# Performance work log

Measured on AMD Instinct MI355X. Metric: run time of the kernel, lower is better.

The kernel has to match this reference:

```python
import jax, jax.numpy as jnp
import numpy as np

N_POINTS = 2_000_000
GRID_SIZE = (256, 256, 256)


def setup_inputs() -> dict:
    key = jax.random.key(0)
    k1, k2 = jax.random.split(key)
    size = jnp.array(GRID_SIZE, dtype=jnp.float32)
    # points uniformly covering the grid so all are valid
    x = jax.random.uniform(k1, (N_POINTS, 3), dtype=jnp.float32) * (size - 1.0)
    grid = jax.random.normal(k2, GRID_SIZE, dtype=jnp.float32)
    lower = jnp.zeros((3,), dtype=jnp.float32)
    resolution = jnp.ones((3,), dtype=jnp.float32)
    return {"x": x, "grid": grid, "lower": lower, "resolution": resolution}


def _corner_mask():
    # mask[k, j] = bit j of corner index k (8 corners of a unit cube)
    return (jnp.arange(8)[:, None] & (1 << jnp.arange(3))[None, :]) != 0  # [8,3] bool


def reference(x, grid, lower, resolution):
    # x: [N,3] points; grid: [nx,ny,nz] learned reflectance grid
    size = jnp.array(grid.shape, dtype=x.dtype)
    index = (x - lower) / resolution                                   # [N,3]
    valid = jnp.all((index >= 0) & (index <= size - 1), axis=-1)       # [N]

    lo = jnp.floor(index)
    hi = jnp.ceil(index)
    mask = _corner_mask()                                              # [8,3]

    # corner coordinates: pick ceil where mask bit set, else floor
    corners = jnp.where(mask[None], hi[:, None, :], lo[:, None, :])    # [N,8,3]
    ci = corners.astype(jnp.int32)
    values = grid[ci[..., 0], ci[..., 1], ci[..., 2]]                  # [N,8] gather

    # weight of each corner = product of distances to the OPPOSITE corner
    opposite = jnp.where(mask[None], lo[:, None, :], hi[:, None, :])   # [N,8,3]
    dist = jnp.abs(opposite - index[:, None, :])                       # [N,8,3]
    dist = dist + (dist == 0).astype(dist.dtype)  # degenerate (integer-coord) axes
    weights = jnp.prod(dist, axis=-1)                                  # [N,8]

    out = jnp.sum(values * weights, axis=-1) / jnp.sum(weights, axis=-1)  # [N]
    return jnp.where(valid, out, jnp.zeros((), dtype=out.dtype))
```

## Files before the change

### kernel.cpp

```cpp
#include <hip/hip_runtime.h>


#define NBINS 1024
#define SPTS 4096
#define SPPT 8

#define RX 17
#define RYZ 1089
#define RN (RX * RYZ)

#define ITHREADS 1024
#define CSTRIDE 16

__device__ __forceinline__ float interp_one(float ix, float iy, float iz,
                                            const float* __restrict__ g,
                                            bool& valid) {
    valid = (ix >= 0.0f) && (ix <= 255.0f) &&
            (iy >= 0.0f) && (iy <= 255.0f) &&
            (iz >= 0.0f) && (iz <= 255.0f);
    if (!valid) return 0.0f;

    float flx = floorf(ix), fcx = ceilf(ix);
    float fly = floorf(iy), fcy = ceilf(iy);
    float flz = floorf(iz), fcz = ceilf(iz);

    int x0 = (int)flx, x1 = (int)fcx;
    int y0 = (int)fly, y1 = (int)fcy;
    int z0 = (int)flz, z1 = (int)fcz;

    float wsx = ix - flx; if (wsx == 0.0f) wsx = 1.0f;
    float wux = fcx - ix; if (wux == 0.0f) wux = 1.0f;
    float wsy = iy - fly; if (wsy == 0.0f) wsy = 1.0f;
    float wuy = fcy - iy; if (wuy == 0.0f) wuy = 1.0f;
    float wsz = iz - flz; if (wsz == 0.0f) wsz = 1.0f;
    float wuz = fcz - iz; if (wuz == 0.0f) wuz = 1.0f;

    int bx0 = x0 << 16, bx1 = x1 << 16;
    int by0 = y0 << 8,  by1 = y1 << 8;

    float v0 = g[bx0 + by0 + z0];  float w0 = wux * wuy * wuz;
    float v1 = g[bx1 + by0 + z0];  float w1 = wsx * wuy * wuz;
    float v2 = g[bx0 + by1 + z0];  float w2 = wux * wsy * wuz;
    float v3 = g[bx1 + by1 + z0];  float w3 = wsx * wsy * wuz;
    float v4 = g[bx0 + by0 + z1];  float w4 = wux * wuy * wsz;
    float v5 = g[bx1 + by0 + z1];  float w5 = wsx * wuy * wsz;
    float v6 = g[bx0 + by1 + z1];  float w6 = wux * wsy * wsz;
    float v7 = g[bx1 + by1 + z1];  float w7 = wsx * wsy * wsz;

    float num = v0 * w0 + v1 * w1 + v2 * w2 + v3 * w3 +
                v4 * w4 + v5 * w5 + v6 * w6 + v7 * w7;
    float den = w0 + w1 + w2 + w3 + w4 + w5 + w6 + w7;
    return num / den;
}

__device__ __forceinline__ unsigned bin_key(float ix, float iy, float iz) {
    ix = fminf(fmaxf(ix, 0.0f), 255.0f);
    iy = fminf(fmaxf(iy, 0.0f), 255.0f);
    iz = fminf(fmaxf(iz, 0.0f), 255.0f);
    int bx = ((int)ix) >> 4;
    int by = ((int)iy) >> 5;
    int bz = ((int)iz) >> 5;
    return (unsigned)((bx << 6) | (by << 3) | bz);
}

__global__ __launch_bounds__(256) void simplegrid_direct(
    const float* __restrict__ x, const float* __restrict__ grid,
    const float* __restrict__ lower, const float* __restrict__ res,
    float* __restrict__ out, int n)
{
    int i = blockIdx.x * blockDim.x + threadIdx.x;
    if (i >= n) return;
    float ix = (x[3 * i + 0] - lower[0]) / res[0];
    float iy = (x[3 * i + 1] - lower[1]) / res[1];
    float iz = (x[3 * i + 2] - lower[2]) / res[2];
    bool valid;
    float v = interp_one(ix, iy, iz, grid, valid);
    out[i] = valid ? v : 0.0f;
}

__global__ __launch_bounds__(512) void init_cursor_kernel(
    unsigned* __restrict__ cursor, unsigned cap)
{
    int t = blockIdx.x * 512 + threadIdx.x;
    if (t < NBINS) cursor[(size_t)t * CSTRIDE] = (unsigned)t * cap;
}

__global__ __launch_bounds__(512) void scatter_kernel(
    const float* __restrict__ x, const float* __restrict__ lower,
    const float* __restrict__ res, unsigned* __restrict__ cursor,
    float* __restrict__ p3, unsigned* __restrict__ posbuf, int n)
{
    __shared__ float sxl[SPTS], syl[SPTS], szl[SPTS];
    __shared__ unsigned short kyl[SPTS];
    __shared__ unsigned cnt[NBINS], pfx[NBINS], lcur[NBINS], gbase[NBINS];
    __shared__ unsigned wsum[8];

    int t = threadIdx.x;
    int lane = t & 63, wave = t >> 6;
    cnt[2 * t] = 0u; cnt[2 * t + 1] = 0u;
    __syncthreads();

    float l0 = lower[0], l1 = lower[1], l2 = lower[2];
    float r0 = res[0],   r1 = res[1],   r2 = res[2];
    int base = blockIdx.x * SPTS;

    float px[SPPT], py[SPPT], pz[SPPT];
    unsigned key[SPPT];
    #pragma unroll
    for (int k = 0; k < SPPT; ++k) {
        int p = base + k * 512 + t;
        if (p < n) {
            px[k] = (x[3 * p + 0] - l0) / r0;
            py[k] = (x[3 * p + 1] - l1) / r1;
            pz[k] = (x[3 * p + 2] - l2) / r2;
            key[k] = bin_key(px[k], py[k], pz[k]);
            atomicAdd(&cnt[key[k]], 1u);
        }
    }
    __syncthreads();

    unsigned h = ((unsigned)blockIdx.x * 131u) & (NBINS - 1);
    unsigned b0 = (2u * t + h) & (NBINS - 1);
    unsigned b1 = (2u * t + 1u + h) & (NBINS - 1);
    unsigned cb0 = cnt[b0], cb1 = cnt[b1];
    if (cb0) gbase[b0] = atomicAdd(&cursor[(size_t)b0 * CSTRIDE], cb0);
    if (cb1) gbase[b1] = atomicAdd(&cursor[(size_t)b1 * CSTRIDE], cb1);

    unsigned c0 = cnt[2 * t], c1 = cnt[2 * t + 1];
    unsigned v = c0 + c1;
    unsigned s = v;
    #pragma unroll
    for (int off = 1; off < 64; off <<= 1) {
        unsigned u = __shfl_up(s, off);
        if (lane >= off) s += u;
    }
    if (lane == 63) wsum[wave] = s;
    __syncthreads();
    unsigned woff = 0, tot = 0;
    #pragma unroll
    for (int w = 0; w < 8; ++w) { if (w < wave) woff += wsum[w]; tot += wsum[w]; }
    unsigned excl = woff + s - v;
    pfx[2 * t] = excl;          lcur[2 * t] = excl;
    pfx[2 * t + 1] = excl + c0; lcur[2 * t + 1] = excl + c0;
    __syncthreads();

    #pragma unroll
    for (int k = 0; k < SPPT; ++k) {
        int p = base + k * 512 + t;
        if (p < n) {
            unsigned lp = atomicAdd(&lcur[key[k]], 1u);
            sxl[lp] = px[k]; syl[lp] = py[k]; szl[lp] = pz[k];
            kyl[lp] = (unsigned short)key[k];
            posbuf[p] = gbase[key[k]] + (lp - pfx[key[k]]);
        }
    }
    __syncthreads();

    for (unsigned q = t; q < tot; q += 512) {
        unsigned kk = kyl[q];
        unsigned dst = gbase[kk] + (q - pfx[kk]);
        size_t b3 = (size_t)dst * 3;
        p3[b3 + 0] = sxl[q];
        p3[b3 + 1] = syl[q];
        p3[b3 + 2] = szl[q];
    }
}

__global__ __launch_bounds__(ITHREADS) void interp_lds_kernel(
    const float* __restrict__ p3, const float* __restrict__ grid,
    const unsigned* __restrict__ cursor, float* __restrict__ osort,
    unsigned cap)
{
    extern __shared__ float lds[];
    int b = blockIdx.x;
    int t = threadIdx.x;
    int bx0 = (b >> 6) << 4;
    int by0 = ((b >> 3) & 7) << 5;
    int bz0 = (b & 7) << 5;

    for (int i = t; i < RN; i += ITHREADS) {
        int lx = i / RYZ;
        int r  = i - lx * RYZ;
        int ly = r / 33;
        int lz = r - ly * 33;
        int gx = bx0 + lx; if (gx > 255) gx = 255;
        int gy = by0 + ly; if (gy > 255) gy = 255;
        int gz = bz0 + lz; if (gz > 255) gz = 255;
        lds[i] = grid[(gx << 16) + (gy << 8) + gz];
    }
    __syncthreads();

    float fbx = (float)bx0, fby = (float)by0, fbz = (float)bz0;
    unsigned start = (unsigned)b * cap;
    unsigned end   = cursor[(size_t)b * CSTRIDE];

    for (unsigned j = start + t; j < end; j += ITHREADS) {
        size_t b3 = (size_t)j * 3;
        float ix = p3[b3 + 0], iy = p3[b3 + 1], iz = p3[b3 + 2];
        bool valid = (ix >= 0.0f) && (ix <= 255.0f) &&
                     (iy >= 0.0f) && (iy <= 255.0f) &&
                     (iz >= 0.0f) && (iz <= 255.0f);
        float fx = fminf(fmaxf(ix, 0.0f), 255.0f) - fbx;
        float fy = fminf(fmaxf(iy, 0.0f), 255.0f) - fby;
        float fz = fminf(fmaxf(iz, 0.0f), 255.0f) - fbz;

        float flx = floorf(fx), fcx = ceilf(fx);
        float fly = floorf(fy), fcy = ceilf(fy);
        float flz = floorf(fz), fcz = ceilf(fz);
        int x0 = (int)flx, x1 = (int)fcx;
        int y0 = (int)fly, y1 = (int)fcy;
        int z0 = (int)flz, z1 = (int)fcz;

        float wsx = fx - flx; if (wsx == 0.0f) wsx = 1.0f;
        float wux = fcx - fx; if (wux == 0.0f) wux = 1.0f;
        float wsy = fy - fly; if (wsy == 0.0f) wsy = 1.0f;
        float wuy = fcy - fy; if (wuy == 0.0f) wuy = 1.0f;
        float wsz = fz - flz; if (wsz == 0.0f) wsz = 1.0f;
        float wuz = fcz - fz; if (wuz == 0.0f) wuz = 1.0f;

        int ax0 = x0 * RYZ, ax1 = x1 * RYZ;
        int ay0 = y0 * 33,  ay1 = y1 * 33;

        float v0 = lds[ax0 + ay0 + z0];  float w0 = wux * wuy * wuz;
        float v1 = lds[ax1 + ay0 + z0];  float w1 = wsx * wuy * wuz;
        float v2 = lds[ax0 + ay1 + z0];  float w2 = wux * wsy * wuz;
        float v3 = lds[ax1 + ay1 + z0];  float w3 = wsx * wsy * wuz;
        float v4 = lds[ax0 + ay0 + z1];  float w4 = wux * wuy * wsz;
        float v5 = lds[ax1 + ay0 + z1];  float w5 = wsx * wuy * wsz;
        float v6 = lds[ax0 + ay1 + z1];  float w6 = wux * wsy * wsz;
        float v7 = lds[ax1 + ay1 + z1];  float w7 = wsx * wsy * wsz;

        float num = v0 * w0 + v1 * w1 + v2 * w2 + v3 * w3 +
                    v4 * w4 + v5 * w5 + v6 * w6 + v7 * w7;
        float den = w0 + w1 + w2 + w3 + w4 + w5 + w6 + w7;
        osort[j] = valid ? (num / den) : 0.0f;
    }
}

__global__ __launch_bounds__(256) void permute_kernel(
    const float* __restrict__ out_sorted, const unsigned* __restrict__ pos,
    float* __restrict__ out, int n)
{
    int i = blockIdx.x * blockDim.x + threadIdx.x;
    if (i < n) out[i] = out_sorted[pos[i]];
}

extern "C" void kernel_launch(void* const* d_in, const int* in_sizes, int n_in,
                              void* d_out, int out_size, void* d_ws, size_t ws_size,
                              hipStream_t stream) {
    const float* x     = (const float*)d_in[0];
    const float* grid  = (const float*)d_in[1];
    const float* lower = (const float*)d_in[2];
    const float* res   = (const float*)d_in[3];
    float* out = (float*)d_out;

    int n = in_sizes[0] / 3;
    int blocks_pt = (n + 255) / 256;

    size_t fixed = (size_t)NBINS * CSTRIDE * 4 + (size_t)n * 4;
    unsigned cap = 0;
    if (ws_size > fixed) {
        size_t c = (ws_size - fixed) / ((size_t)NBINS * 16);
        cap = (unsigned)(c > 8192 ? 8192 : c);
    }

    bool lds_ok = (hipFuncSetAttribute(
        (const void*)interp_lds_kernel,
        hipFuncAttributeMaxDynamicSharedMemorySize,
        RN * (int)sizeof(float)) == hipSuccess);

    if (cap < 2560 || !lds_ok) {
        simplegrid_direct<<<blocks_pt, 256, 0, stream>>>(x, grid, lower, res, out, n);
        return;
    }

    char* ws = (char*)d_ws;
    size_t off_p3    = (size_t)NBINS * CSTRIDE * 4;
    size_t off_osort = off_p3 + (size_t)NBINS * cap * 12;
    size_t off_pos   = off_osort + (size_t)NBINS * cap * 4;

    unsigned* cursor = (unsigned*)ws;
    float*    p3     = (float*)(ws + off_p3);
    float*    osort  = (float*)(ws + off_osort);
    unsigned* posbuf = (unsigned*)(ws + off_pos);

    int blocks_sort = (n + SPTS - 1) / SPTS;

    init_cursor_kernel<<<2, 512, 0, stream>>>(cursor, cap);
    scatter_kernel<<<blocks_sort, 512, 0, stream>>>(
        x, lower, res, cursor, p3, posbuf, n);
    interp_lds_kernel<<<NBINS, ITHREADS, RN * sizeof(float), stream>>>(
        p3, grid, cursor, osort, cap);
    permute_kernel<<<blocks_pt, 256, 0, stream>>>(osort, posbuf, out, n);
}
```

Baseline: 84.53 us.

## Split bin cursors into sub-bins and pack sorted points as float4

Each of the 1024 spatial bins now gets 16 sub-bin cursors, selected by scatter block index. This spreads the global atomicAdd contention on each bin cursor across 16 addresses. The interpolation kernel rebuilds a contiguous index space over the sub-bin segments with a small prefix sum and a binary search per point. Sorted points are now stored as padded float4 so each point is written and read with a single vector access. The cost is 33% more workspace per slot, per-point search overhead, and a higher workspace threshold (cap >= 4096), which could force the slow direct fallback when workspace is small.

```diff
diff --git a/kernel.cpp b/kernel.cpp
--- a/kernel.cpp
+++ b/kernel.cpp
@@ -2,6 +2,7 @@
 
 
 #define NBINS 1024
+#define NSUB 16
 #define SPTS 4096
 #define SPPT 8
 
@@ -82,13 +83,17 @@
     unsigned* __restrict__ cursor, unsigned cap)
 {
     int t = blockIdx.x * 512 + threadIdx.x;
-    if (t < NBINS) cursor[(size_t)t * CSTRIDE] = (unsigned)t * cap;
+    if (t < NBINS * NSUB) {
+        unsigned s = (unsigned)t >> 10;
+        unsigned b = (unsigned)t & (NBINS - 1);
+        cursor[(size_t)t * CSTRIDE] = b * cap + s * (cap / NSUB);
+    }
 }
 
 __global__ __launch_bounds__(512) void scatter_kernel(
     const float* __restrict__ x, const float* __restrict__ lower,
     const float* __restrict__ res, unsigned* __restrict__ cursor,
-    float* __restrict__ p3, unsigned* __restrict__ posbuf, int n)
+    float4* __restrict__ p4, unsigned* __restrict__ posbuf, int n)
 {
     __shared__ float sxl[SPTS], syl[SPTS], szl[SPTS];
     __shared__ unsigned short kyl[SPTS];
@@ -119,12 +124,13 @@
     }
     __syncthreads();
 
+    unsigned sub = (unsigned)blockIdx.x & (NSUB - 1);
     unsigned h = ((unsigned)blockIdx.x * 131u) & (NBINS - 1);
     unsigned b0 = (2u * t + h) & (NBINS - 1);
     unsigned b1 = (2u * t + 1u + h) & (NBINS - 1);
     unsigned cb0 = cnt[b0], cb1 = cnt[b1];
-    if (cb0) gbase[b0] = atomicAdd(&cursor[(size_t)b0 * CSTRIDE], cb0);
-    if (cb1) gbase[b1] = atomicAdd(&cursor[(size_t)b1 * CSTRIDE], cb1);
+    if (cb0) gbase[b0] = atomicAdd(&cursor[(size_t)((sub << 10) | b0) * CSTRIDE], cb0);
+    if (cb1) gbase[b1] = atomicAdd(&cursor[(size_t)((sub << 10) | b1) * CSTRIDE], cb1);
 
     unsigned c0 = cnt[2 * t], c1 = cnt[2 * t + 1];
     unsigned v = c0 + c1;
@@ -159,24 +165,32 @@
     for (unsigned q = t; q < tot; q += 512) {
         unsigned kk = kyl[q];
         unsigned dst = gbase[kk] + (q - pfx[kk]);
-        size_t b3 = (size_t)dst * 3;
-        p3[b3 + 0] = sxl[q];
-        p3[b3 + 1] = syl[q];
-        p3[b3 + 2] = szl[q];
+        p4[dst] = make_float4(sxl[q], syl[q], szl[q], 0.0f);
     }
 }
 
 __global__ __launch_bounds__(ITHREADS) void interp_lds_kernel(
-    const float* __restrict__ p3, const float* __restrict__ grid,
+    const float4* __restrict__ p4, const float* __restrict__ grid,
     const unsigned* __restrict__ cursor, float* __restrict__ osort,
     unsigned cap)
 {
     extern __shared__ float lds[];
+    __shared__ unsigned sstart[NSUB + 1];
+    __shared__ unsigned sbase[NSUB];
+
     int b = blockIdx.x;
     int t = threadIdx.x;
     int bx0 = (b >> 6) << 4;
     int by0 = ((b >> 3) & 7) << 5;
     int bz0 = (b & 7) << 5;
+
+    if (t < NSUB) {
+        unsigned subcap = cap / NSUB;
+        unsigned st = (unsigned)b * cap + (unsigned)t * subcap;
+        unsigned en = cursor[(size_t)(((unsigned)t << 10) | (unsigned)b) * CSTRIDE];
+        sbase[t] = st;
+        sstart[t] = en - st;
+    }
 
     for (int i = t; i < RN; i += ITHREADS) {
         int lx = i / RYZ;
@@ -190,13 +204,32 @@
     }
     __syncthreads();
 
+    if (t == 0) {
+        unsigned acc = 0;
+        #pragma unroll
+        for (int s2 = 0; s2 < NSUB; ++s2) {
+            unsigned c = sstart[s2];
+            sstart[s2] = acc;
+            acc += c;
+        }
+        sstart[NSUB] = acc;
+    }
+    __syncthreads();
+
     float fbx = (float)bx0, fby = (float)by0, fbz = (float)bz0;
-    unsigned start = (unsigned)b * cap;
-    unsigned end   = cursor[(size_t)b * CSTRIDE];
-
-    for (unsigned j = start + t; j < end; j += ITHREADS) {
-        size_t b3 = (size_t)j * 3;
-        float ix = p3[b3 + 0], iy = p3[b3 + 1], iz = p3[b3 + 2];
+    unsigned tot = sstart[NSUB];
+
+    for (unsigned idx = t; idx < tot; idx += ITHREADS) {
+        unsigned lo = 0, hi = NSUB;
+        #pragma unroll
+        for (int it = 0; it < 4; ++it) {
+            unsigned mid = (lo + hi) >> 1;
+            if (sstart[mid] <= idx) lo = mid; else hi = mid;
+        }
+        unsigned j = sbase[lo] + (idx - sstart[lo]);
+
+        float4 p = p4[j];
+        float ix = p.x, iy = p.y, iz = p.z;
         bool valid = (ix >= 0.0f) && (ix <= 255.0f) &&
                      (iy >= 0.0f) && (iy <= 255.0f) &&
                      (iz >= 0.0f) && (iz <= 255.0f);
@@ -257,11 +290,13 @@
     int n = in_sizes[0] / 3;
     int blocks_pt = (n + 255) / 256;
 
-    size_t fixed = (size_t)NBINS * CSTRIDE * 4 + (size_t)n * 4;
+    size_t cur_bytes = (size_t)NBINS * NSUB * CSTRIDE * 4;
+    size_t fixed = cur_bytes + (size_t)n * 4;
     unsigned cap = 0;
     if (ws_size > fixed) {
-        size_t c = (ws_size - fixed) / ((size_t)NBINS * 16);
+        size_t c = (ws_size - fixed) / ((size_t)NBINS * 20);
         cap = (unsigned)(c > 8192 ? 8192 : c);
+        cap &= ~(unsigned)(NSUB - 1);
     }
 
     bool lds_ok = (hipFuncSetAttribute(
@@ -269,27 +304,27 @@
         hipFuncAttributeMaxDynamicSharedMemorySize,
         RN * (int)sizeof(float)) == hipSuccess);
 
-    if (cap < 2560 || !lds_ok) {
+    if (cap < 4096 || !lds_ok) {
         simplegrid_direct<<<blocks_pt, 256, 0, stream>>>(x, grid, lower, res, out, n);
         return;
     }
 
     char* ws = (char*)d_ws;
-    size_t off_p3    = (size_t)NBINS * CSTRIDE * 4;
-    size_t off_osort = off_p3 + (size_t)NBINS * cap * 12;
+    size_t off_p4    = cur_bytes;
+    size_t off_osort = off_p4 + (size_t)NBINS * cap * 16;
     size_t off_pos   = off_osort + (size_t)NBINS * cap * 4;
 
     unsigned* cursor = (unsigned*)ws;
-    float*    p3     = (float*)(ws + off_p3);
+    float4*   p4     = (float4*)(ws + off_p4);
     float*    osort  = (float*)(ws + off_osort);
     unsigned* posbuf = (unsigned*)(ws + off_pos);
 
     int blocks_sort = (n + SPTS - 1) / SPTS;
 
-    init_cursor_kernel<<<2, 512, 0, stream>>>(cursor, cap);
+    init_cursor_kernel<<<32, 512, 0, stream>>>(cursor, cap);
     scatter_kernel<<<blocks_sort, 512, 0, stream>>>(
-        x, lower, res, cursor, p3, posbuf, n);
+        x, lower, res, cursor, p4, posbuf, n);
     interp_lds_kernel<<<NBINS, ITHREADS, RN * sizeof(float), stream>>>(
-        p3, grid, cursor, osort, cap);
+        p4, grid, cursor, osort, cap);
     permute_kernel<<<blocks_pt, 256, 0, stream>>>(osort, posbuf, out, n);
 }
```

Measured after the change: 85.99 us. Within noise of the previous version (+1.7%).

## Scatter point indices instead of coordinates and regather x in interp

Applied to the files above, without the earlier changes.

The scatter kernel now writes only a 4-byte point index per sorted slot instead of three floats staged through LDS. The interpolation kernel gathers each point's coordinates from x through that index. Scatter blocks grow to 1024 threads over 8192 points, and the per-bin capacity is capped at 4096. This cuts scatter write traffic and LDS staging, but turns the interp kernel's coalesced coordinate reads into random gathers from x. The lower capacity cap could push some workspace sizes onto the fallback path or overflow bins.

```diff
diff --git a/kernel.cpp b/kernel.cpp
--- a/kernel.cpp
+++ b/kernel.cpp
@@ -2,7 +2,7 @@
 
 
 #define NBINS 1024
-#define SPTS 4096
+#define SPTS 8192
 #define SPPT 8
 
 #define RX 17
@@ -85,49 +85,45 @@
     if (t < NBINS) cursor[(size_t)t * CSTRIDE] = (unsigned)t * cap;
 }
 
-__global__ __launch_bounds__(512) void scatter_kernel(
+__global__ __launch_bounds__(1024) void scatter_kernel(
     const float* __restrict__ x, const float* __restrict__ lower,
     const float* __restrict__ res, unsigned* __restrict__ cursor,
-    float* __restrict__ p3, unsigned* __restrict__ posbuf, int n)
-{
-    __shared__ float sxl[SPTS], syl[SPTS], szl[SPTS];
-    __shared__ unsigned short kyl[SPTS];
+    unsigned* __restrict__ ord, unsigned* __restrict__ posbuf, int n)
+{
     __shared__ unsigned cnt[NBINS], pfx[NBINS], lcur[NBINS], gbase[NBINS];
-    __shared__ unsigned wsum[8];
+    __shared__ unsigned wsum[16];
 
     int t = threadIdx.x;
     int lane = t & 63, wave = t >> 6;
-    cnt[2 * t] = 0u; cnt[2 * t + 1] = 0u;
+    cnt[t] = 0u;
     __syncthreads();
 
     float l0 = lower[0], l1 = lower[1], l2 = lower[2];
     float r0 = res[0],   r1 = res[1],   r2 = res[2];
     int base = blockIdx.x * SPTS;
 
-    float px[SPPT], py[SPPT], pz[SPPT];
     unsigned key[SPPT];
     #pragma unroll
     for (int k = 0; k < SPPT; ++k) {
-        int p = base + k * 512 + t;
+        int p = base + k * 1024 + t;
         if (p < n) {
-            px[k] = (x[3 * p + 0] - l0) / r0;
-            py[k] = (x[3 * p + 1] - l1) / r1;
-            pz[k] = (x[3 * p + 2] - l2) / r2;
-            key[k] = bin_key(px[k], py[k], pz[k]);
+            float ix = (x[3 * p + 0] - l0) / r0;
+            float iy = (x[3 * p + 1] - l1) / r1;
+            float iz = (x[3 * p + 2] - l2) / r2;
+            key[k] = bin_key(ix, iy, iz);
             atomicAdd(&cnt[key[k]], 1u);
+        } else {
+            key[k] = 0xFFFFFFFFu;
         }
     }
     __syncthreads();
 
     unsigned h = ((unsigned)blockIdx.x * 131u) & (NBINS - 1);
-    unsigned b0 = (2u * t + h) & (NBINS - 1);
-    unsigned b1 = (2u * t + 1u + h) & (NBINS - 1);
-    unsigned cb0 = cnt[b0], cb1 = cnt[b1];
-    if (cb0) gbase[b0] = atomicAdd(&cursor[(size_t)b0 * CSTRIDE], cb0);
-    if (cb1) gbase[b1] = atomicAdd(&cursor[(size_t)b1 * CSTRIDE], cb1);
-
-    unsigned c0 = cnt[2 * t], c1 = cnt[2 * t + 1];
-    unsigned v = c0 + c1;
+    unsigned br = ((unsigned)t + h) & (NBINS - 1);
+    unsigned cb = cnt[br];
+    if (cb) gbase[br] = atomicAdd(&cursor[(size_t)br * CSTRIDE], cb);
+
+    unsigned v = cnt[t];
     unsigned s = v;
     #pragma unroll
     for (int off = 1; off < 64; off <<= 1) {
@@ -136,40 +132,32 @@
     }
     if (lane == 63) wsum[wave] = s;
     __syncthreads();
-    unsigned woff = 0, tot = 0;
-    #pragma unroll
-    for (int w = 0; w < 8; ++w) { if (w < wave) woff += wsum[w]; tot += wsum[w]; }
+    unsigned woff = 0;
+    #pragma unroll
+    for (int w = 0; w < 16; ++w) if (w < wave) woff += wsum[w];
     unsigned excl = woff + s - v;
-    pfx[2 * t] = excl;          lcur[2 * t] = excl;
-    pfx[2 * t + 1] = excl + c0; lcur[2 * t + 1] = excl + c0;
+    pfx[t] = excl;
+    lcur[t] = excl;
     __syncthreads();
 
     #pragma unroll
     for (int k = 0; k < SPPT; ++k) {
-        int p = base + k * 512 + t;
+        int p = base + k * 1024 + t;
         if (p < n) {
-            unsigned lp = atomicAdd(&lcur[key[k]], 1u);
-            sxl[lp] = px[k]; syl[lp] = py[k]; szl[lp] = pz[k];
-            kyl[lp] = (unsigned short)key[k];
-            posbuf[p] = gbase[key[k]] + (lp - pfx[key[k]]);
+            unsigned kk = key[k];
+            unsigned lp = atomicAdd(&lcur[kk], 1u);
+            unsigned dst = gbase[kk] + (lp - pfx[kk]);
+            posbuf[p] = dst;
+            ord[dst] = (unsigned)p;
         }
     }
-    __syncthreads();
-
-    for (unsigned q = t; q < tot; q += 512) {
-        unsigned kk = kyl[q];
-        unsigned dst = gbase[kk] + (q - pfx[kk]);
-        size_t b3 = (size_t)dst * 3;
-        p3[b3 + 0] = sxl[q];
-        p3[b3 + 1] = syl[q];
-        p3[b3 + 2] = szl[q];
-    }
 }
 
 __global__ __launch_bounds__(ITHREADS) void interp_lds_kernel(
-    const float* __restrict__ p3, const float* __restrict__ grid,
-    const unsigned* __restrict__ cursor, float* __restrict__ osort,
-    unsigned cap)
+    const unsigned* __restrict__ ord, const float* __restrict__ x,
+    const float* __restrict__ lower, const float* __restrict__ res,
+    const float* __restrict__ grid, const unsigned* __restrict__ cursor,
+    float* __restrict__ osort, unsigned cap)
 {
     extern __shared__ float lds[];
     int b = blockIdx.x;
@@ -190,13 +178,17 @@
     }
     __syncthreads();
 
+    float l0 = lower[0], l1 = lower[1], l2 = lower[2];
+    float r0 = res[0],   r1 = res[1],   r2 = res[2];
     float fbx = (float)bx0, fby = (float)by0, fbz = (float)bz0;
     unsigned start = (unsigned)b * cap;
     unsigned end   = cursor[(size_t)b * CSTRIDE];
 
     for (unsigned j = start + t; j < end; j += ITHREADS) {
-        size_t b3 = (size_t)j * 3;
-        float ix = p3[b3 + 0], iy = p3[b3 + 1], iz = p3[b3 + 2];
+        unsigned o = ord[j];
+        float ix = (x[3 * o + 0] - l0) / r0;
+        float iy = (x[3 * o + 1] - l1) / r1;
+        float iz = (x[3 * o + 2] - l2) / r2;
         bool valid = (ix >= 0.0f) && (ix <= 255.0f) &&
                      (iy >= 0.0f) && (iy <= 255.0f) &&
                      (iz >= 0.0f) && (iz <= 255.0f);
@@ -257,11 +249,12 @@
     int n = in_sizes[0] / 3;
     int blocks_pt = (n + 255) / 256;
 
-    size_t fixed = (size_t)NBINS * CSTRIDE * 4 + (size_t)n * 4;
+    size_t cur_bytes = (size_t)NBINS * CSTRIDE * 4;
+    size_t fixed = cur_bytes + (size_t)n * 4;
     unsigned cap = 0;
     if (ws_size > fixed) {
-        size_t c = (ws_size - fixed) / ((size_t)NBINS * 16);
-        cap = (unsigned)(c > 8192 ? 8192 : c);
+        size_t c = (ws_size - fixed) / ((size_t)NBINS * 8);
+        cap = (unsigned)(c > 4096 ? 4096 : c);
     }
 
     bool lds_ok = (hipFuncSetAttribute(
@@ -275,21 +268,21 @@
     }
 
     char* ws = (char*)d_ws;
-    size_t off_p3    = (size_t)NBINS * CSTRIDE * 4;
-    size_t off_osort = off_p3 + (size_t)NBINS * cap * 12;
+    size_t off_ord   = cur_bytes;
+    size_t off_osort = off_ord + (size_t)NBINS * cap * 4;
     size_t off_pos   = off_osort + (size_t)NBINS * cap * 4;
 
     unsigned* cursor = (unsigned*)ws;
-    float*    p3     = (float*)(ws + off_p3);
+    unsigned* ord    = (unsigned*)(ws + off_ord);
     float*    osort  = (float*)(ws + off_osort);
     unsigned* posbuf = (unsigned*)(ws + off_pos);
 
     int blocks_sort = (n + SPTS - 1) / SPTS;
 
     init_cursor_kernel<<<2, 512, 0, stream>>>(cursor, cap);
-    scatter_kernel<<<blocks_sort, 512, 0, stream>>>(
-        x, lower, res, cursor, p3, posbuf, n);
+    scatter_kernel<<<blocks_sort, 1024, 0, stream>>>(
+        x, lower, res, cursor, ord, posbuf, n);
     interp_lds_kernel<<<NBINS, ITHREADS, RN * sizeof(float), stream>>>(
-        p3, grid, cursor, osort, cap);
+        ord, x, lower, res, grid, cursor, osort, cap);
     permute_kernel<<<blocks_pt, 256, 0, stream>>>(osort, posbuf, out, n);
 }
```

Measured after the change: 110.3 us. 1.31x slower.
